# Kernel tuning notes

Measured on AMD Instinct MI355X. Metric: run time of the kernel, lower is better.

Reference implementation:

```python
import jax, jax.numpy as jnp
import numpy as np

HIDDEN = 2048
HEAD_DIM = 128
N_HEADS = 16
N_KV_HEADS = 8
Q_DIM = N_HEADS * HEAD_DIM          # 2048
K_DIM = N_KV_HEADS * HEAD_DIM       # 1024
ROPE_THETA = 1.0e6
EPS = 1e-6
T = 4096


def setup_inputs() -> dict:
    key = jax.random.key(0)
    ks = jax.random.split(key, 4)
    x = jax.random.normal(ks[0], (T, HIDDEN), dtype=jnp.float32)
    qkv_w = jax.random.normal(ks[1], (Q_DIM + 2 * K_DIM, HIDDEN), dtype=jnp.float32) * 0.02
    o_w = jax.random.normal(ks[2], (HIDDEN, Q_DIM), dtype=jnp.float32) * 0.02
    q_norm_w = jnp.ones((HEAD_DIM,), dtype=jnp.float32)
    k_norm_w = jnp.ones((HEAD_DIM,), dtype=jnp.float32)
    positions = jnp.arange(T, dtype=jnp.int64 if jax.config.jax_enable_x64 else jnp.int32)
    return {"x": x, "qkv_w": qkv_w, "q_norm_w": q_norm_w,
            "k_norm_w": k_norm_w, "o_w": o_w, "positions": positions}


def _rms_norm(v, w):
    # v: [T, H, D]; normalize over last dim
    var = jnp.mean(v * v, axis=-1, keepdims=True)
    return v * jax.lax.rsqrt(var + EPS) * w


def _rope(v, cos, sin):
    # neox style: rotate halves. v: [T, H, D]; cos/sin: [T, 1, D/2]
    half = v.shape[-1] // 2
    v1, v2 = v[..., :half], v[..., half:]
    return jnp.concatenate([v1 * cos - v2 * sin, v2 * cos + v1 * sin], axis=-1)


def reference(x, qkv_w, q_norm_w, k_norm_w, o_w, positions):
    t = x.shape[0]
    qkv = x @ qkv_w.T                                   # [T, Q_DIM+2*K_DIM]
    q = qkv[:, :Q_DIM].reshape(t, N_HEADS, HEAD_DIM)
    k = qkv[:, Q_DIM:Q_DIM + K_DIM].reshape(t, N_KV_HEADS, HEAD_DIM)
    v = qkv[:, Q_DIM + K_DIM:].reshape(t, N_KV_HEADS, HEAD_DIM)

    q = _rms_norm(q, q_norm_w)
    k = _rms_norm(k, k_norm_w)

    half = HEAD_DIM // 2
    inv_freq = 1.0 / (ROPE_THETA ** (jnp.arange(0, half, dtype=jnp.float32) / half))
    freqs = positions.astype(jnp.float32)[:, None] * inv_freq[None, :]  # [T, half]
    cos = jnp.cos(freqs)[:, None, :]                     # [T, 1, half]
    sin = jnp.sin(freqs)[:, None, :]
    q = _rope(q, cos, sin)
    k = _rope(k, cos, sin)

    # GQA: each kv head serves N_HEADS // N_KV_HEADS query heads
    rep = N_HEADS // N_KV_HEADS
    k = jnp.repeat(k, rep, axis=1)                       # [T, N_HEADS, D]
    v = jnp.repeat(v, rep, axis=1)

    scale = 1.0 / np.sqrt(HEAD_DIM)
    scores = jnp.einsum('thd,shd->hts', q, k) * scale    # [H, T, T]
    causal = positions[:, None] >= positions[None, :]    # [T, T]
    scores = jnp.where(causal[None, :, :], scores, jnp.float32(-1e9))
    attn = jax.nn.softmax(scores, axis=-1)
    o = jnp.einsum('hts,shd->thd', attn, v)              # [T, H, D]
    o = o.reshape(t, Q_DIM)
    return o @ o_w.T                                     # [T, HIDDEN]
```

## Files before the change

kernel.cpp:

```cpp
#include <hip/hip_runtime.h>

#define Tq   4096
#define HIDN 2048
#define NHEAD 16
#define NKV  8
#define DH   128
#define QKVN 4096

typedef unsigned short u16;
typedef unsigned int   u32;
typedef __attribute__((ext_vector_type(8))) __bf16 bf16x8;
typedef __attribute__((ext_vector_type(8))) u16    u16x8;
typedef __attribute__((ext_vector_type(4))) float  f32x4;

#define GLD16(gp, lp) __builtin_amdgcn_global_load_lds( \
    (const __attribute__((address_space(1))) void*)(gp), \
    (__attribute__((address_space(3))) void*)(lp), 16, 0, 0)

__device__ __forceinline__ u16 f2bf(float f) {
  union { float f; u32 u; } v; v.f = f;
  return (u16)((v.u + 0x7fffu + ((v.u >> 16) & 1u)) >> 16);
}
__device__ __forceinline__ float bf2f(u32 bits) {
  union { u32 u; float f; } v; v.u = bits << 16;
  return v.f;
}

__global__ __launch_bounds__(256) void cast_bf16_kernel(const float* __restrict__ in,
                                                        u16* __restrict__ out, int n) {
  int i = (blockIdx.x * 256 + threadIdx.x) * 8;
  if (i >= n) return;
  f32x4 a = *(const f32x4*)(in + i);
  f32x4 b = *(const f32x4*)(in + i + 4);
  u16x8 o;
  #pragma unroll
  for (int j = 0; j < 4; ++j) { o[j] = f2bf(a[j]); o[4 + j] = f2bf(b[j]); }
  *(u16x8*)(out + i) = o;
}

template<bool OUT_BF16>
__global__ __launch_bounds__(256) void gemm_bt_kernel(const u16* __restrict__ A,
                                                      const u16* __restrict__ B,
                                                      void* __restrict__ Cout,
                                                      int M, int N, int K) {
  __shared__ u16 As[128 * 32];
  __shared__ u16 Bs[128 * 32];
  const int tid = threadIdx.x;
  const int lane = tid & 63, wv = tid >> 6;
  const int wr = wv >> 1, wc = wv & 1;
  const int g = lane >> 4, c = lane & 15;
  const int nbn = N >> 7;
  const int bm = blockIdx.x / nbn, bn = blockIdx.x % nbn;
  const int m0 = bm << 7, n0 = bn << 7;

  const int srow = tid >> 2;
  const int sk8 = (tid & 3) * 8;
  const u16* gA0 = A + (size_t)(m0 + srow) * K + sk8;
  const u16* gA1 = gA0 + (size_t)64 * K;
  const u16* gB0 = B + (size_t)(n0 + srow) * K + sk8;
  const u16* gB1 = gB0 + (size_t)64 * K;
  u16* lA0 = As + (wv * 64) * 8;
  u16* lA1 = As + (wv * 64 + 256) * 8;
  u16* lB0 = Bs + (wv * 64) * 8;
  u16* lB1 = Bs + (wv * 64 + 256) * 8;

  f32x4 acc[4][4] = {};

  for (int kt = 0; kt < K; kt += 32) {
    __syncthreads();
    GLD16(gA0 + kt, lA0); GLD16(gA1 + kt, lA1);
    GLD16(gB0 + kt, lB0); GLD16(gB1 + kt, lB1);
    __syncthreads();
    bf16x8 af[4], bfr[4];
    #pragma unroll
    for (int mi = 0; mi < 4; ++mi)
      af[mi] = *(const bf16x8*)&As[(wr * 64 + mi * 16 + c) * 32 + g * 8];
    #pragma unroll
    for (int ni = 0; ni < 4; ++ni)
      bfr[ni] = *(const bf16x8*)&Bs[(wc * 64 + ni * 16 + c) * 32 + g * 8];
    #pragma unroll
    for (int mi = 0; mi < 4; ++mi)
      #pragma unroll
      for (int ni = 0; ni < 4; ++ni)
        acc[mi][ni] = __builtin_amdgcn_mfma_f32_16x16x32_bf16(af[mi], bfr[ni], acc[mi][ni], 0, 0, 0);
  }

  #pragma unroll
  for (int mi = 0; mi < 4; ++mi)
    #pragma unroll
    for (int ni = 0; ni < 4; ++ni) {
      const int row = m0 + wr * 64 + mi * 16 + 4 * g;
      const int col = n0 + wc * 64 + ni * 16 + c;
      #pragma unroll
      for (int j = 0; j < 4; ++j) {
        if (OUT_BF16) ((u16*)Cout)[(size_t)(row + j) * N + col] = f2bf(acc[mi][ni][j]);
        else          ((float*)Cout)[(size_t)(row + j) * N + col] = acc[mi][ni][j];
      }
    }
}

__global__ __launch_bounds__(256) void normrope_kernel(u16* __restrict__ qkv,
                                                       const float* __restrict__ qw,
                                                       const float* __restrict__ kw) {
  const int tid = threadIdx.x, lane = tid & 63, wv = tid >> 6;
  const int wid = blockIdx.x * 4 + wv;
  const int t = wid / 24;
  const int hh = wid % 24;
  const int off = (hh < 16) ? hh * DH : 2048 + (hh - 16) * DH;
  const float* w = (hh < 16) ? qw : kw;
  u16* base = qkv + (size_t)t * QKVN + off;
  const int d0 = lane * 2;

  u32 raw = *(const u32*)(base + d0);
  float v0 = bf2f(raw & 0xffffu), v1 = bf2f(raw >> 16);
  float ss = v0 * v0 + v1 * v1;
  #pragma unroll
  for (int m = 1; m <= 32; m <<= 1) ss += __shfl_xor(ss, m);
  const float rn = rsqrtf(ss * (1.0f / 128.0f) + 1e-6f);
  float n0 = v0 * rn * w[d0];
  float n1 = v1 * rn * w[d0 + 1];
  float o0 = __shfl_xor(n0, 32);
  float o1 = __shfl_xor(n1, 32);
  const int j0 = (lane & 31) * 2;
  const float p = (float)t;
  const float lf = 0.31143075889568947f;
  float a0 = p * __builtin_exp2f(-lf * (float)j0);
  float a1 = p * __builtin_exp2f(-lf * (float)(j0 + 1));
  float c0 = cosf(a0), s0 = sinf(a0), c1 = cosf(a1), s1 = sinf(a1);
  float r0, r1;
  if (lane < 32) { r0 = n0 * c0 - o0 * s0; r1 = n1 * c1 - o1 * s1; }
  else           { r0 = n0 * c0 + o0 * s0; r1 = n1 * c1 + o1 * s1; }
  *(u32*)(base + d0) = (u32)f2bf(r0) | ((u32)f2bf(r1) << 16);
}

__global__ __launch_bounds__(256) void vtrans_kernel(const u16* __restrict__ qkv,
                                                     u16* __restrict__ vt) {
  __shared__ u16 tile[64][72];
  const int tid = threadIdx.x;
  const int b = blockIdx.x;
  const int kvh = b >> 7;
  const int r = b & 127;
  const int t0 = (r & 63) * 64;
  const int d0 = (r >> 6) * 64;
  #pragma unroll
  for (int i = 0; i < 2; ++i) {
    int cidx = tid + i * 256;
    int trow = cidx >> 3, dcol = (cidx & 7) * 8;
    u16x8 v = *(const u16x8*)&qkv[(size_t)(t0 + trow) * QKVN + 3072 + kvh * DH + d0 + dcol];
    *(u16x8*)&tile[trow][dcol] = v;
  }
  __syncthreads();
  #pragma unroll
  for (int i = 0; i < 2; ++i) {
    int cidx = tid + i * 256;
    int drow = cidx >> 3, tcol = (cidx & 7) * 8;
    u16x8 v;
    #pragma unroll
    for (int j = 0; j < 8; ++j) v[j] = tile[tcol + j][drow];
    *(u16x8*)&vt[(size_t)kvh * DH * Tq + (size_t)(d0 + drow) * Tq + t0 + tcol] = v;
  }
}

__global__ __launch_bounds__(512) void attn2_kernel(const u16* __restrict__ qkv,
                                                    const u16* __restrict__ vt,
                                                    u16* __restrict__ o) {
  __shared__ u16 Ks[64 * 128];
  __shared__ u16 Vs[128 * 64];
  __shared__ u16 Ps[8][16][72];
  const int tid = threadIdx.x, lane = tid & 63, wv = tid >> 6;
  const int g = lane >> 4, c = lane & 15;
  const int bid = blockIdx.x;
  const int qt = (bid < 256) ? (31 - (bid >> 4)) : ((bid - 256) >> 4);
  const int head = bid & 15;
  const int kvh = head >> 1;
  const int qblk0 = qt * 128;
  const int q0w = qblk0 + wv * 16;
  const float c2 = 0.08838834764831845f * 1.4426950408889634f;

  int koff[2], voff[2];
  #pragma unroll
  for (int j = 0; j < 2; ++j) {
    int i = j * 512 + wv * 64 + lane;
    int kr = i >> 4, kcc = i & 15;
    koff[j] = kr * QKVN + 2048 + kvh * DH + ((kcc ^ (kr & 7)) * 8);
    int vr = i >> 3, vcc = i & 7;
    voff[j] = vr * Tq + ((vcc ^ (vr & 7)) * 8);
  }
  const u16* vbase_g = vt + (size_t)kvh * DH * Tq;
  const int xk = c & 7;

  bf16x8 qf[4];
  #pragma unroll
  for (int ks = 0; ks < 4; ++ks)
    qf[ks] = *(const bf16x8*)&qkv[(size_t)(q0w + c) * QKVN + head * DH + ks * 32 + g * 8];

  f32x4 oacc[8] = {};
  float mrow[4] = { -3e38f, -3e38f, -3e38f, -3e38f };
  float lrow[4] = { 0.f, 0.f, 0.f, 0.f };

  const int nkvb = qt * 2 + 2;
  for (int kb = 0; kb < nkvb; ++kb) {
    const int kv0 = kb * 64;
    __syncthreads();
    #pragma unroll
    for (int j = 0; j < 2; ++j) {
      GLD16(qkv + (size_t)kv0 * QKVN + koff[j], Ks + (j * 512 + wv * 64) * 8);
      GLD16(vbase_g + kv0 + voff[j],           Vs + (j * 512 + wv * 64) * 8);
    }
    __syncthreads();
    if (kv0 <= q0w + 15) {
      f32x4 s[4] = {};
      #pragma unroll
      for (int st = 0; st < 4; ++st)
        #pragma unroll
        for (int ks = 0; ks < 4; ++ks) {
          bf16x8 kf = *(const bf16x8*)&Ks[(st * 16 + c) * 128 + (((ks * 4 + g) ^ xk) * 8)];
          s[st] = __builtin_amdgcn_mfma_f32_16x16x32_bf16(qf[ks], kf, s[st], 0, 0, 0);
        }
      if (kv0 + 63 > q0w) {
        #pragma unroll
        for (int st = 0; st < 4; ++st) {
          const int kvc = kv0 + st * 16 + c;
          #pragma unroll
          for (int j = 0; j < 4; ++j)
            if (kvc > q0w + 4 * g + j) s[st][j] = -1e9f;
        }
      }
      #pragma unroll
      for (int j = 0; j < 4; ++j) {
        float mx = fmaxf(fmaxf(s[0][j], s[1][j]), fmaxf(s[2][j], s[3][j]));
        mx = fmaxf(mx, __shfl_xor(mx, 1));
        mx = fmaxf(mx, __shfl_xor(mx, 2));
        mx = fmaxf(mx, __shfl_xor(mx, 4));
        mx = fmaxf(mx, __shfl_xor(mx, 8));
        const float mn = fmaxf(mrow[j], mx);
        const float alpha = __builtin_exp2f(c2 * (mrow[j] - mn));
        mrow[j] = mn;
        lrow[j] *= alpha;
        float ps = 0.f;
        #pragma unroll
        for (int st = 0; st < 4; ++st) {
          float pv = __builtin_exp2f(c2 * (s[st][j] - mn));
          s[st][j] = pv;
          ps += pv;
        }
        ps += __shfl_xor(ps, 1); ps += __shfl_xor(ps, 2);
        ps += __shfl_xor(ps, 4); ps += __shfl_xor(ps, 8);
        lrow[j] += ps;
        #pragma unroll
        for (int db = 0; db < 8; ++db) oacc[db][j] *= alpha;
      }
      #pragma unroll
      for (int st = 0; st < 4; ++st)
        #pragma unroll
        for (int j = 0; j < 4; ++j)
          Ps[wv][4 * g + j][st * 16 + c] = f2bf(s[st][j]);
      bf16x8 pa0 = *(const bf16x8*)&Ps[wv][c][g * 8];
      bf16x8 pa1 = *(const bf16x8*)&Ps[wv][c][32 + g * 8];
      #pragma unroll
      for (int db = 0; db < 8; ++db) {
        bf16x8 vf0 = *(const bf16x8*)&Vs[(db * 16 + c) * 64 + ((g ^ xk) * 8)];
        oacc[db] = __builtin_amdgcn_mfma_f32_16x16x32_bf16(pa0, vf0, oacc[db], 0, 0, 0);
        bf16x8 vf1 = *(const bf16x8*)&Vs[(db * 16 + c) * 64 + (((4 + g) ^ xk) * 8)];
        oacc[db] = __builtin_amdgcn_mfma_f32_16x16x32_bf16(pa1, vf1, oacc[db], 0, 0, 0);
      }
    }
  }
  #pragma unroll
  for (int j = 0; j < 4; ++j) lrow[j] = 1.0f / lrow[j];
  #pragma unroll
  for (int db = 0; db < 8; ++db)
    #pragma unroll
    for (int j = 0; j < 4; ++j)
      o[(size_t)(q0w + 4 * g + j) * HIDN + head * DH + db * 16 + c] = f2bf(oacc[db][j] * lrow[j]);
}

extern "C" void kernel_launch(void* const* d_in, const int* in_sizes, int n_in,
                              void* d_out, int out_size, void* d_ws, size_t ws_size,
                              hipStream_t stream) {
  const float* x    = (const float*)d_in[0];
  const float* qkvw = (const float*)d_in[1];
  const float* qnw  = (const float*)d_in[2];
  const float* knw  = (const float*)d_in[3];
  const float* ow   = (const float*)d_in[4];

  char* ws = (char*)d_ws;
  u16* xb   = (u16*)ws;
  u16* wb   = (u16*)(ws + (16u << 20));
  u16* qkvb = (u16*)(ws + (32u << 20));
  u16* vtb  = (u16*)(ws + (64u << 20));
  u16* owb  = xb;
  u16* ob   = wb;

  cast_bf16_kernel<<<4096, 256, 0, stream>>>(x,    xb, Tq * HIDN);
  cast_bf16_kernel<<<4096, 256, 0, stream>>>(qkvw, wb, QKVN * HIDN);
  gemm_bt_kernel<true><<<1024, 256, 0, stream>>>(xb, wb, (void*)qkvb, Tq, QKVN, HIDN);
  normrope_kernel<<<24576, 256, 0, stream>>>(qkvb, qnw, knw);
  vtrans_kernel<<<1024, 256, 0, stream>>>(qkvb, vtb);
  cast_bf16_kernel<<<2048, 256, 0, stream>>>(ow, owb, HIDN * HIDN);
  attn2_kernel<<<512, 512, 0, stream>>>(qkvb, vtb, ob);
  gemm_bt_kernel<false><<<512, 256, 0, stream>>>(ob, owb, d_out, Tq, HIDN, HIDN);
}
```

Baseline: 519.3 us.

## Rewrite attention with paired causal tiles, register prefetch, lazy rescale, MFMA row sums

The attention kernel now gives each block two mirrored query tiles (p and 31-p), which balances causal work across 256 blocks. K/V tiles are prefetched into registers while the current tile is computed, replacing direct global-to-LDS loads. Softmax rescaling is skipped unless the row max grows by more than a threshold. Row sums come from an extra ones-row in V folded into the MFMA, and packed bf16 conversion uses an inline asm instruction. The trade-off is more register pressure, an extra MFMA tile per step, and reliance on the threshold staying numerically safe.

```diff
diff --git a/kernel.cpp b/kernel.cpp
--- a/kernel.cpp
+++ b/kernel.cpp
@@ -161,118 +161,153 @@
   }
 }
 
-__global__ __launch_bounds__(512) void attn2_kernel(const u16* __restrict__ qkv,
+__global__ __launch_bounds__(512) void attn3_kernel(const u16* __restrict__ qkv,
                                                     const u16* __restrict__ vt,
                                                     u16* __restrict__ o) {
   __shared__ u16 Ks[64 * 128];
-  __shared__ u16 Vs[128 * 64];
+  __shared__ u16 Vs[144 * 64];
   __shared__ u16 Ps[8][16][72];
   const int tid = threadIdx.x, lane = tid & 63, wv = tid >> 6;
   const int g = lane >> 4, c = lane & 15;
   const int bid = blockIdx.x;
-  const int qt = (bid < 256) ? (31 - (bid >> 4)) : ((bid - 256) >> 4);
   const int head = bid & 15;
+  const int p = bid >> 4;
   const int kvh = head >> 1;
-  const int qblk0 = qt * 128;
-  const int q0w = qblk0 + wv * 16;
   const float c2 = 0.08838834764831845f * 1.4426950408889634f;
-
-  int koff[2], voff[2];
+  const float THR = 40.0f;
+  const int xk = c & 7;
+
+  for (int i = tid; i < 16 * 64; i += 512) Vs[128 * 64 + i] = (i < 64) ? 0x3F80 : 0;
+
+  int kOff[2], kDst[2], vOff[2], vDst[2];
   #pragma unroll
   for (int j = 0; j < 2; ++j) {
     int i = j * 512 + wv * 64 + lane;
     int kr = i >> 4, kcc = i & 15;
-    koff[j] = kr * QKVN + 2048 + kvh * DH + ((kcc ^ (kr & 7)) * 8);
+    kOff[j] = kr * QKVN + 2048 + kvh * DH + kcc * 8;
+    kDst[j] = kr * 128 + ((kcc ^ (kr & 7)) * 8);
     int vr = i >> 3, vcc = i & 7;
-    voff[j] = vr * Tq + ((vcc ^ (vr & 7)) * 8);
-  }
-  const u16* vbase_g = vt + (size_t)kvh * DH * Tq;
-  const int xk = c & 7;
-
-  bf16x8 qf[4];
-  #pragma unroll
-  for (int ks = 0; ks < 4; ++ks)
-    qf[ks] = *(const bf16x8*)&qkv[(size_t)(q0w + c) * QKVN + head * DH + ks * 32 + g * 8];
-
-  f32x4 oacc[8] = {};
-  float mrow[4] = { -3e38f, -3e38f, -3e38f, -3e38f };
-  float lrow[4] = { 0.f, 0.f, 0.f, 0.f };
-
-  const int nkvb = qt * 2 + 2;
-  for (int kb = 0; kb < nkvb; ++kb) {
-    const int kv0 = kb * 64;
-    __syncthreads();
+    vOff[j] = vr * Tq + vcc * 8;
+    vDst[j] = vr * 64 + ((vcc ^ (vr & 7)) * 8);
+  }
+  const u16* vkv = vt + (size_t)kvh * DH * Tq;
+  u16x8 kreg[2], vreg[2];
+
+  #pragma unroll 1
+  for (int seg = 0; seg < 2; ++seg) {
+    const int qt = seg ? (31 - p) : p;
+    const int q0w = qt * 128 + wv * 16;
+    const int nkvb = qt * 2 + 2;
+
+    bf16x8 qf[4];
+    #pragma unroll
+    for (int ks = 0; ks < 4; ++ks)
+      qf[ks] = *(const bf16x8*)&qkv[(size_t)(q0w + c) * QKVN + head * DH + ks * 32 + g * 8];
+
+    f32x4 oacc[9] = {};
+    float mrow[4] = { -3e38f, -3e38f, -3e38f, -3e38f };
+
     #pragma unroll
     for (int j = 0; j < 2; ++j) {
-      GLD16(qkv + (size_t)kv0 * QKVN + koff[j], Ks + (j * 512 + wv * 64) * 8);
-      GLD16(vbase_g + kv0 + voff[j],           Vs + (j * 512 + wv * 64) * 8);
+      kreg[j] = *(const u16x8*)(qkv + kOff[j]);
+      vreg[j] = *(const u16x8*)(vkv + vOff[j]);
     }
-    __syncthreads();
-    if (kv0 <= q0w + 15) {
-      f32x4 s[4] = {};
+
+    for (int kb = 0; kb < nkvb; ++kb) {
+      const int kv0 = kb * 64;
       #pragma unroll
-      for (int st = 0; st < 4; ++st)
-        #pragma unroll
-        for (int ks = 0; ks < 4; ++ks) {
-          bf16x8 kf = *(const bf16x8*)&Ks[(st * 16 + c) * 128 + (((ks * 4 + g) ^ xk) * 8)];
-          s[st] = __builtin_amdgcn_mfma_f32_16x16x32_bf16(qf[ks], kf, s[st], 0, 0, 0);
-        }
-      if (kv0 + 63 > q0w) {
+      for (int j = 0; j < 2; ++j) {
+        *(u16x8*)&Ks[kDst[j]] = kreg[j];
+        *(u16x8*)&Vs[vDst[j]] = vreg[j];
+      }
+      __syncthreads();
+      {
+        const int kvn = (kb + 1 < nkvb) ? (kv0 + 64) : kv0;
+        #pragma unroll
+        for (int j = 0; j < 2; ++j) {
+          kreg[j] = *(const u16x8*)(qkv + (size_t)kvn * QKVN + kOff[j]);
+          vreg[j] = *(const u16x8*)(vkv + kvn + vOff[j]);
+        }
+      }
+      if (kv0 <= q0w + 15) {
+        f32x4 s[4] = {};
+        #pragma unroll
+        for (int st = 0; st < 4; ++st)
+          #pragma unroll
+          for (int ks = 0; ks < 4; ++ks) {
+            bf16x8 kf = *(const bf16x8*)&Ks[(st * 16 + c) * 128 + (((ks * 4 + g) ^ xk) * 8)];
+            s[st] = __builtin_amdgcn_mfma_f32_16x16x32_bf16(qf[ks], kf, s[st], 0, 0, 0);
+          }
+        if (kv0 + 63 > q0w) {
+          #pragma unroll
+          for (int st = 0; st < 4; ++st) {
+            const int kvc = kv0 + st * 16 + c;
+            #pragma unroll
+            for (int j = 0; j < 4; ++j)
+              if (kvc > q0w + 4 * g + j) s[st][j] = -1e9f;
+          }
+        }
+        float mx[4];
+        int need = 0;
+        #pragma unroll
+        for (int j = 0; j < 4; ++j) {
+          float m3 = fmaxf(fmaxf(s[0][j], s[1][j]), fmaxf(s[2][j], s[3][j]));
+          m3 = fmaxf(m3, __shfl_xor(m3, 1));
+          m3 = fmaxf(m3, __shfl_xor(m3, 2));
+          m3 = fmaxf(m3, __shfl_xor(m3, 4));
+          m3 = fmaxf(m3, __shfl_xor(m3, 8));
+          mx[j] = m3;
+          need |= (m3 > mrow[j] + THR);
+        }
+        if (__any(need)) {
+          #pragma unroll
+          for (int j = 0; j < 4; ++j) {
+            const float mn = fmaxf(mrow[j], mx[j]);
+            const float alpha = __builtin_exp2f(c2 * (mrow[j] - mn));
+            mrow[j] = mn;
+            #pragma unroll
+            for (int db = 0; db < 9; ++db) oacc[db][j] *= alpha;
+          }
+        }
+        #pragma unroll
+        for (int j = 0; j < 4; ++j) {
+          const float cm = c2 * mrow[j];
+          #pragma unroll
+          for (int st = 0; st < 4; ++st)
+            s[st][j] = __builtin_exp2f(c2 * s[st][j] - cm);
+        }
         #pragma unroll
         for (int st = 0; st < 4; ++st) {
-          const int kvc = kv0 + st * 16 + c;
-          #pragma unroll
-          for (int j = 0; j < 4; ++j)
-            if (kvc > q0w + 4 * g + j) s[st][j] = -1e9f;
+          u32 pk01, pk23;
+          asm("v_cvt_pk_bf16_f32 %0, %1, %2" : "=v"(pk01) : "v"(s[st][0]), "v"(s[st][1]));
+          asm("v_cvt_pk_bf16_f32 %0, %1, %2" : "=v"(pk23) : "v"(s[st][2]), "v"(s[st][3]));
+          Ps[wv][4 * g + 0][st * 16 + c] = (u16)pk01;
+          Ps[wv][4 * g + 1][st * 16 + c] = (u16)(pk01 >> 16);
+          Ps[wv][4 * g + 2][st * 16 + c] = (u16)pk23;
+          Ps[wv][4 * g + 3][st * 16 + c] = (u16)(pk23 >> 16);
+        }
+        bf16x8 pa0 = *(const bf16x8*)&Ps[wv][c][g * 8];
+        bf16x8 pa1 = *(const bf16x8*)&Ps[wv][c][32 + g * 8];
+        #pragma unroll
+        for (int db = 0; db < 9; ++db) {
+          bf16x8 vf0 = *(const bf16x8*)&Vs[(db * 16 + c) * 64 + ((g ^ xk) * 8)];
+          oacc[db] = __builtin_amdgcn_mfma_f32_16x16x32_bf16(pa0, vf0, oacc[db], 0, 0, 0);
+          bf16x8 vf1 = *(const bf16x8*)&Vs[(db * 16 + c) * 64 + (((4 + g) ^ xk) * 8)];
+          oacc[db] = __builtin_amdgcn_mfma_f32_16x16x32_bf16(pa1, vf1, oacc[db], 0, 0, 0);
         }
       }
+      __syncthreads();
+    }
+
+    #pragma unroll
+    for (int j = 0; j < 4; ++j) {
+      const float ls = __shfl(oacc[8][j], lane & 48);
+      const float inv = 1.0f / ls;
       #pragma unroll
-      for (int j = 0; j < 4; ++j) {
-        float mx = fmaxf(fmaxf(s[0][j], s[1][j]), fmaxf(s[2][j], s[3][j]));
-        mx = fmaxf(mx, __shfl_xor(mx, 1));
-        mx = fmaxf(mx, __shfl_xor(mx, 2));
-        mx = fmaxf(mx, __shfl_xor(mx, 4));
-        mx = fmaxf(mx, __shfl_xor(mx, 8));
-        const float mn = fmaxf(mrow[j], mx);
-        const float alpha = __builtin_exp2f(c2 * (mrow[j] - mn));
-        mrow[j] = mn;
-        lrow[j] *= alpha;
-        float ps = 0.f;
-        #pragma unroll
-        for (int st = 0; st < 4; ++st) {
-          float pv = __builtin_exp2f(c2 * (s[st][j] - mn));
-          s[st][j] = pv;
-          ps += pv;
-        }
-        ps += __shfl_xor(ps, 1); ps += __shfl_xor(ps, 2);
-        ps += __shfl_xor(ps, 4); ps += __shfl_xor(ps, 8);
-        lrow[j] += ps;
-        #pragma unroll
-        for (int db = 0; db < 8; ++db) oacc[db][j] *= alpha;
-      }
-      #pragma unroll
-      for (int st = 0; st < 4; ++st)
-        #pragma unroll
-        for (int j = 0; j < 4; ++j)
-          Ps[wv][4 * g + j][st * 16 + c] = f2bf(s[st][j]);
-      bf16x8 pa0 = *(const bf16x8*)&Ps[wv][c][g * 8];
-      bf16x8 pa1 = *(const bf16x8*)&Ps[wv][c][32 + g * 8];
-      #pragma unroll
-      for (int db = 0; db < 8; ++db) {
-        bf16x8 vf0 = *(const bf16x8*)&Vs[(db * 16 + c) * 64 + ((g ^ xk) * 8)];
-        oacc[db] = __builtin_amdgcn_mfma_f32_16x16x32_bf16(pa0, vf0, oacc[db], 0, 0, 0);
-        bf16x8 vf1 = *(const bf16x8*)&Vs[(db * 16 + c) * 64 + (((4 + g) ^ xk) * 8)];
-        oacc[db] = __builtin_amdgcn_mfma_f32_16x16x32_bf16(pa1, vf1, oacc[db], 0, 0, 0);
-      }
+      for (int db = 0; db < 8; ++db)
+        o[(size_t)(q0w + 4 * g + j) * HIDN + head * DH + db * 16 + c] = f2bf(oacc[db][j] * inv);
     }
   }
-  #pragma unroll
-  for (int j = 0; j < 4; ++j) lrow[j] = 1.0f / lrow[j];
-  #pragma unroll
-  for (int db = 0; db < 8; ++db)
-    #pragma unroll
-    for (int j = 0; j < 4; ++j)
-      o[(size_t)(q0w + 4 * g + j) * HIDN + head * DH + db * 16 + c] = f2bf(oacc[db][j] * lrow[j]);
 }
 
 extern "C" void kernel_launch(void* const* d_in, const int* in_sizes, int n_in,
@@ -298,6 +333,6 @@
   normrope_kernel<<<24576, 256, 0, stream>>>(qkvb, qnw, knw);
   vtrans_kernel<<<1024, 256, 0, stream>>>(qkvb, vtb);
   cast_bf16_kernel<<<2048, 256, 0, stream>>>(ow, owb, HIDN * HIDN);
-  attn2_kernel<<<512, 512, 0, stream>>>(qkvb, vtb, ob);
+  attn3_kernel<<<256, 512, 0, stream>>>(qkvb, vtb, ob);
   gemm_bt_kernel<false><<<512, 256, 0, stream>>>(ob, owb, d_out, Tq, HIDN, HIDN);
 }
```

Result: faster. 456.9 us (-12.0%).
